# Performance work log

Hardware: AMD Instinct MI355X
Metric: run time of the kernel (lower is better)

Reference implementation:

```python
import jax, jax.numpy as jnp
import numpy as np

EPS = 1e-8


def setup_inputs() -> dict:
    key = jax.random.key(0)
    k1, k2, k3, k4, k5 = jax.random.split(key, 5)
    B, N_LOG, N_PHYS, E = 16, 512, 2048, 2048
    P = jax.random.uniform(k1, (B, N_LOG, N_PHYS), dtype=jnp.float32)
    d_hw = jax.random.randint(k2, (N_PHYS, N_PHYS), 0, 4, dtype=jnp.int32)
    edge_src = jax.random.randint(k3, (B, E), 0, N_LOG, dtype=jnp.int32)
    edge_dst = jax.random.randint(k4, (B, E), 0, N_LOG, dtype=jnp.int32)
    edge_w = jax.random.uniform(k5, (B, E), dtype=jnp.float32)
    return {"P": P, "d_hw": d_hw, "edge_src": edge_src,
            "edge_dst": edge_dst, "edge_w": edge_w}


def reference(P, d_hw, edge_src, edge_dst, edge_w):
    # A_hw[p,q] = 1 where hardware distance == 1 (adjacent qubits)
    A_hw = (d_hw == 1).astype(P.dtype)                      # [Q, Q]
    B = P.shape[0]
    # Dense contraction once per batch: PA[b,i,q] = sum_p P[b,i,p] A[p,q]
    PA = jnp.einsum('bip,pq->biq', P, A_hw)                 # [B, N, Q]
    b_idx = jnp.arange(B)[:, None]                          # [B, 1]
    gi = PA[b_idx, edge_src]                                # [B, E, Q]
    gj = P[b_idx, edge_dst]                                 # [B, E, Q]
    adj_score = jnp.einsum('beq,beq->be', gi, gj)           # [B, E]
    sample_adj = jnp.sum(edge_w * adj_score, axis=-1)       # [B]
    sample_weight = jnp.maximum(jnp.sum(edge_w, axis=-1), EPS)
    # every sample has edges -> valid_samples = B
    loss = -jnp.mean(sample_adj / sample_weight)
    return loss
```

## Files before the change

### kernel.cpp

```cpp
#include <hip/hip_runtime.h>
#include <hip/hip_bf16.h>

#define BATCH 16
#define NLOG 512
#define Q 2048
#define NEDGE 2048
#define M_TOT (BATCH * NLOG)
#define KB 2048

typedef float f32x4 __attribute__((ext_vector_type(4)));
typedef int i32x4 __attribute__((ext_vector_type(4)));
typedef int i32x8 __attribute__((ext_vector_type(8)));

__device__ __forceinline__ unsigned char to_e4m3(float f) {
    int pk = __builtin_amdgcn_cvt_pk_fp8_f32(f, f, 0, false);
    return (unsigned char)(pk & 0xff);
}

__global__ __launch_bounds__(256) void prep(const float* __restrict__ P,
                                            unsigned char* __restrict__ P8,
                                            const int* __restrict__ d_hw,
                                            unsigned char* __restrict__ A8t,
                                            unsigned* __restrict__ counter) {
    int bid = blockIdx.x;
    if (bid == 0 && threadIdx.x == 0) *counter = 0u;
    if (bid < 8192) {
        int i = (bid * 256 + threadIdx.x) * 8;
        float4 v0 = *(const float4*)(P + i);
        float4 v1 = *(const float4*)(P + i + 4);
        int lo = 0, hi = 0;
        lo = __builtin_amdgcn_cvt_pk_fp8_f32(v0.x, v0.y, lo, false);
        lo = __builtin_amdgcn_cvt_pk_fp8_f32(v0.z, v0.w, lo, true);
        hi = __builtin_amdgcn_cvt_pk_fp8_f32(v1.x, v1.y, hi, false);
        hi = __builtin_amdgcn_cvt_pk_fp8_f32(v1.z, v1.w, hi, true);
        int2 st; st.x = lo; st.y = hi;
        *(int2*)(P8 + i) = st;
    } else {
        bid -= 8192;
        __shared__ unsigned char tile[32][33];
        int q0 = (bid & 63) * 32;
        int p0 = (bid >> 6) * 32;
        int tx = threadIdx.x & 31;
        int ty = threadIdx.x >> 5;
        for (int s = 0; s < 32; s += 8) {
            int p = p0 + ty + s;
            int v = d_hw[(size_t)p * Q + q0 + tx];
            tile[ty + s][tx] = (v == 1) ? 0x38 : 0x00;
        }
        __syncthreads();
        for (int s = 0; s < 32; s += 8) {
            A8t[(size_t)(q0 + ty + s) * Q + p0 + tx] = tile[tx][ty + s];
        }
    }
}

__global__ __launch_bounds__(256, 2) void gemm_bt8(const unsigned char* __restrict__ A,
                                                   const unsigned char* __restrict__ Bt,
                                                   unsigned char* __restrict__ PA8) {
    __shared__ unsigned char As[32768];
    __shared__ unsigned char Bs[16384];

    const int t = threadIdx.x;
    const int w = t >> 6;
    const int wr = w >> 1, wc = w & 1;
    const int l = t & 63;
    const int quad = l >> 4;
    const int lane16 = l & 15;

    const int m0 = blockIdx.x * 256;
    const int n0 = blockIdx.y * 128;

    const int s_row = t >> 3;
    const int s_off = (((t & 7) ^ (s_row & 7)) << 4);

    const int r7 = lane16 & 7;
    const int c0 = ((2 * quad) ^ r7) << 4;
    const int c1 = ((2 * quad + 1) ^ r7) << 4;

    f32x4 acc[8][4] = {};

    for (int k0 = 0; k0 < KB; k0 += 128) {
        #pragma unroll
        for (int c = 0; c < 8; c++) {
            const unsigned char* g = A + (size_t)(m0 + c * 32 + s_row) * KB + k0 + s_off;
            __builtin_amdgcn_global_load_lds(
                (const __attribute__((address_space(1))) void*)g,
                (__attribute__((address_space(3))) void*)(As + c * 4096 + w * 1024),
                16, 0, 0);
        }
        #pragma unroll
        for (int c = 0; c < 4; c++) {
            const unsigned char* g = Bt + (size_t)(n0 + c * 32 + s_row) * KB + k0 + s_off;
            __builtin_amdgcn_global_load_lds(
                (const __attribute__((address_space(1))) void*)g,
                (__attribute__((address_space(3))) void*)(Bs + c * 4096 + w * 1024),
                16, 0, 0);
        }
        __syncthreads();

        i32x8 bfr[4];
        #pragma unroll
        for (int j = 0; j < 4; j++) {
            int base = (wc * 64 + j * 16 + lane16) << 7;
            i32x4 lo = *(const i32x4*)(Bs + base + c0);
            i32x4 hi = *(const i32x4*)(Bs + base + c1);
            bfr[j] = __builtin_shufflevector(lo, hi, 0, 1, 2, 3, 4, 5, 6, 7);
        }
        #pragma unroll
        for (int i = 0; i < 8; i++) {
            int base = (wr * 128 + i * 16 + lane16) << 7;
            i32x4 lo = *(const i32x4*)(As + base + c0);
            i32x4 hi = *(const i32x4*)(As + base + c1);
            i32x8 af = __builtin_shufflevector(lo, hi, 0, 1, 2, 3, 4, 5, 6, 7);
            #pragma unroll
            for (int j = 0; j < 4; j++)
                acc[i][j] = __builtin_amdgcn_mfma_scale_f32_16x16x128_f8f6f4(
                    af, bfr[j], acc[i][j], 0, 0,
                    0, 127,
                    0, 127);
        }
        __syncthreads();
    }

    #pragma unroll
    for (int i = 0; i < 8; i++) {
        #pragma unroll
        for (int j = 0; j < 4; j++) {
            #pragma unroll
            for (int r = 0; r < 4; r++) {
                int row = m0 + wr * 128 + i * 16 + quad * 4 + r;
                int col = n0 + wc * 64 + j * 16 + lane16;
                PA8[(size_t)row * Q + col] = to_e4m3(acc[i][j][r] * (1.0f / 256.0f));
            }
        }
    }
}

__global__ __launch_bounds__(256, 2) void gemm_s8(const unsigned char* __restrict__ PA8,
                                                  const unsigned char* __restrict__ P8,
                                                  __hip_bfloat16* __restrict__ S) {
    __shared__ unsigned char As[8192];
    __shared__ unsigned char Bs[16384];

    const int t = threadIdx.x;
    const int w = t >> 6;
    const int wr = w >> 1, wc = w & 1;
    const int l = t & 63;
    const int quad = l >> 4;
    const int lane16 = l & 15;

    const int b = blockIdx.z;
    const int m0 = blockIdx.x * 64;
    const int n0 = blockIdx.y * 128;
    const unsigned char* A  = PA8 + (size_t)b * NLOG * Q;
    const unsigned char* Bt = P8  + (size_t)b * NLOG * Q;
    __hip_bfloat16* C = S + (size_t)b * NLOG * NLOG;

    const int s_row = t >> 3;
    const int s_off = (((t & 7) ^ (s_row & 7)) << 4);
    const int r7 = lane16 & 7;
    const int c0 = ((2 * quad) ^ r7) << 4;
    const int c1 = ((2 * quad + 1) ^ r7) << 4;

    f32x4 acc[2][4] = {};

    for (int k0 = 0; k0 < KB; k0 += 128) {
        #pragma unroll
        for (int c = 0; c < 2; c++) {
            const unsigned char* g = A + (size_t)(m0 + c * 32 + s_row) * KB + k0 + s_off;
            __builtin_amdgcn_global_load_lds(
                (const __attribute__((address_space(1))) void*)g,
                (__attribute__((address_space(3))) void*)(As + c * 4096 + w * 1024),
                16, 0, 0);
        }
        #pragma unroll
        for (int c = 0; c < 4; c++) {
            const unsigned char* g = Bt + (size_t)(n0 + c * 32 + s_row) * KB + k0 + s_off;
            __builtin_amdgcn_global_load_lds(
                (const __attribute__((address_space(1))) void*)g,
                (__attribute__((address_space(3))) void*)(Bs + c * 4096 + w * 1024),
                16, 0, 0);
        }
        __syncthreads();

        i32x8 bfr[4];
        #pragma unroll
        for (int j = 0; j < 4; j++) {
            int base = (wc * 64 + j * 16 + lane16) << 7;
            i32x4 lo = *(const i32x4*)(Bs + base + c0);
            i32x4 hi = *(const i32x4*)(Bs + base + c1);
            bfr[j] = __builtin_shufflevector(lo, hi, 0, 1, 2, 3, 4, 5, 6, 7);
        }
        #pragma unroll
        for (int i = 0; i < 2; i++) {
            int base = (wr * 32 + i * 16 + lane16) << 7;
            i32x4 lo = *(const i32x4*)(As + base + c0);
            i32x4 hi = *(const i32x4*)(As + base + c1);
            i32x8 af = __builtin_shufflevector(lo, hi, 0, 1, 2, 3, 4, 5, 6, 7);
            #pragma unroll
            for (int j = 0; j < 4; j++)
                acc[i][j] = __builtin_amdgcn_mfma_scale_f32_16x16x128_f8f6f4(
                    af, bfr[j], acc[i][j], 0, 0, 0, 127, 0, 127);
        }
        __syncthreads();
    }

    #pragma unroll
    for (int i = 0; i < 2; i++) {
        #pragma unroll
        for (int j = 0; j < 4; j++) {
            #pragma unroll
            for (int r = 0; r < 4; r++) {
                int row = m0 + wr * 32 + i * 16 + quad * 4 + r;
                int col = n0 + wc * 64 + j * 16 + lane16;
                C[(size_t)row * NLOG + col] = __float2bfloat16(acc[i][j][r]);
            }
        }
    }
}

__global__ __launch_bounds__(256) void edge_final(const __hip_bfloat16* __restrict__ S,
                                                  const int* __restrict__ esrc,
                                                  const int* __restrict__ edst,
                                                  const float* __restrict__ ew,
                                                  float* __restrict__ adj,
                                                  float* __restrict__ wsum,
                                                  unsigned* __restrict__ counter,
                                                  float* __restrict__ out) {
    const int b = blockIdx.x;
    const int t = threadIdx.x;
    const unsigned short* Sb = (const unsigned short*)S + (size_t)b * NLOG * NLOG;
    float a = 0.f, ws = 0.f;
    #pragma unroll
    for (int k = 0; k < NEDGE / 256; k++) {
        int e = b * NEDGE + k * 256 + t;
        int src = esrc[e];
        int dst = edst[e];
        float wg = ew[e];
        float s = __uint_as_float((unsigned)Sb[src * NLOG + dst] << 16) * 256.0f;
        a += wg * s;
        ws += wg;
    }
    #pragma unroll
    for (int off = 32; off > 0; off >>= 1) {
        a += __shfl_xor(a, off);
        ws += __shfl_xor(ws, off);
    }
    __shared__ float ra[4], rw[4];
    if ((t & 63) == 0) { ra[t >> 6] = a; rw[t >> 6] = ws; }
    __syncthreads();

    __shared__ unsigned done;
    if (t == 0) {
        atomicExch(&adj[b],  ra[0] + ra[1] + ra[2] + ra[3]);
        atomicExch(&wsum[b], rw[0] + rw[1] + rw[2] + rw[3]);
        __threadfence();
        done = atomicAdd(counter, 1u);
    }
    __syncthreads();
    if (done == BATCH - 1 && t == 0) {
        __threadfence();
        float s = 0.f;
        #pragma unroll
        for (int bb = 0; bb < BATCH; bb++) {
            float av = atomicAdd(&adj[bb], 0.0f);
            float wv = atomicAdd(&wsum[bb], 0.0f);
            s += av / fmaxf(wv, 1e-8f);
        }
        out[0] = -s / (float)BATCH;
    }
}

extern "C" void kernel_launch(void* const* d_in, const int* in_sizes, int n_in,
                              void* d_out, int out_size, void* d_ws, size_t ws_size,
                              hipStream_t stream) {
    const float* P    = (const float*)d_in[0];
    const int* d_hw   = (const int*)d_in[1];
    const int* esrc   = (const int*)d_in[2];
    const int* edst   = (const int*)d_in[3];
    const float* ew   = (const float*)d_in[4];
    float* out        = (float*)d_out;

    char* ws = (char*)d_ws;
    unsigned char* P8  = (unsigned char*)ws;
    unsigned char* A8t = (unsigned char*)(ws + 16777216);
    unsigned char* PA8 = (unsigned char*)(ws + 20971520);
    __hip_bfloat16* S  = (__hip_bfloat16*)(ws + 37748736);
    float* adj         = (float*)(ws + 46137344);
    float* wsum        = (float*)(ws + 46137344 + 64);
    unsigned* counter  = (unsigned*)(ws + 46137344 + 128);

    prep<<<8192 + 4096, 256, 0, stream>>>(P, P8, d_hw, A8t, counter);
    gemm_bt8<<<dim3(M_TOT / 256, Q / 128), 256, 0, stream>>>(P8, A8t, PA8);
    gemm_s8<<<dim3(NLOG / 64, NLOG / 128, BATCH), 256, 0, stream>>>(PA8, P8, S);
    edge_final<<<BATCH, 256, 0, stream>>>(S, esrc, edst, ew, adj, wsum, counter, out);
}
```

Before: 183.1 us.

## Replace dense per-batch S GEMM with direct per-edge gathered dot products

Drops the full 512x512 per-batch S = PA·Pᵀ GEMM and the S buffer. Each edge now gathers its PA row and P row and computes their dot product on the fp8 MFMA, keeping only the diagonal of each 16x16 output tile. Blocks accumulate into adj/wsum with atomicAdd, and the last of 512 blocks computes the final loss. This removes the N²·Q GEMM work in exchange for about 2x redundant row gathers per edge and diagonal-only MFMA use.

```diff
diff --git a/kernel.cpp b/kernel.cpp
--- a/kernel.cpp
+++ b/kernel.cpp
@@ -21,9 +21,14 @@
                                             unsigned char* __restrict__ P8,
                                             const int* __restrict__ d_hw,
                                             unsigned char* __restrict__ A8t,
+                                            float* __restrict__ adj,
+                                            float* __restrict__ wsum,
                                             unsigned* __restrict__ counter) {
     int bid = blockIdx.x;
-    if (bid == 0 && threadIdx.x == 0) *counter = 0u;
+    if (bid == 0) {
+        if (threadIdx.x == 0) *counter = 0u;
+        if (threadIdx.x < BATCH) { adj[threadIdx.x] = 0.f; wsum[threadIdx.x] = 0.f; }
+    }
     if (bid < 8192) {
         int i = (bid * 256 + threadIdx.x) * 8;
         float4 v0 = *(const float4*)(P + i);
@@ -136,129 +141,77 @@
     }
 }
 
-__global__ __launch_bounds__(256, 2) void gemm_s8(const unsigned char* __restrict__ PA8,
-                                                  const unsigned char* __restrict__ P8,
-                                                  __hip_bfloat16* __restrict__ S) {
-    __shared__ unsigned char As[8192];
-    __shared__ unsigned char Bs[16384];
-
+__global__ __launch_bounds__(256, 2) void edge_dot(const unsigned char* __restrict__ PA8,
+                                                   const unsigned char* __restrict__ P8,
+                                                   const int* __restrict__ esrc,
+                                                   const int* __restrict__ edst,
+                                                   const float* __restrict__ ew,
+                                                   float* __restrict__ adj,
+                                                   float* __restrict__ wsum,
+                                                   unsigned* __restrict__ counter,
+                                                   float* __restrict__ out) {
+    const int lid = blockIdx.x;
+    const int b   = (lid & 7) | ((lid >> 8) << 3);
+    const int bx  = (lid >> 3) & 31;
     const int t = threadIdx.x;
     const int w = t >> 6;
-    const int wr = w >> 1, wc = w & 1;
-    const int l = t & 63;
-    const int quad = l >> 4;
-    const int lane16 = l & 15;
-
-    const int b = blockIdx.z;
-    const int m0 = blockIdx.x * 64;
-    const int n0 = blockIdx.y * 128;
-    const unsigned char* A  = PA8 + (size_t)b * NLOG * Q;
-    const unsigned char* Bt = P8  + (size_t)b * NLOG * Q;
-    __hip_bfloat16* C = S + (size_t)b * NLOG * NLOG;
-
-    const int s_row = t >> 3;
-    const int s_off = (((t & 7) ^ (s_row & 7)) << 4);
-    const int r7 = lane16 & 7;
-    const int c0 = ((2 * quad) ^ r7) << 4;
-    const int c1 = ((2 * quad + 1) ^ r7) << 4;
-
-    f32x4 acc[2][4] = {};
-
-    for (int k0 = 0; k0 < KB; k0 += 128) {
-        #pragma unroll
-        for (int c = 0; c < 2; c++) {
-            const unsigned char* g = A + (size_t)(m0 + c * 32 + s_row) * KB + k0 + s_off;
-            __builtin_amdgcn_global_load_lds(
-                (const __attribute__((address_space(1))) void*)g,
-                (__attribute__((address_space(3))) void*)(As + c * 4096 + w * 1024),
-                16, 0, 0);
-        }
-        #pragma unroll
-        for (int c = 0; c < 4; c++) {
-            const unsigned char* g = Bt + (size_t)(n0 + c * 32 + s_row) * KB + k0 + s_off;
-            __builtin_amdgcn_global_load_lds(
-                (const __attribute__((address_space(1))) void*)g,
-                (__attribute__((address_space(3))) void*)(Bs + c * 4096 + w * 1024),
-                16, 0, 0);
-        }
-        __syncthreads();
-
-        i32x8 bfr[4];
-        #pragma unroll
-        for (int j = 0; j < 4; j++) {
-            int base = (wc * 64 + j * 16 + lane16) << 7;
-            i32x4 lo = *(const i32x4*)(Bs + base + c0);
-            i32x4 hi = *(const i32x4*)(Bs + base + c1);
-            bfr[j] = __builtin_shufflevector(lo, hi, 0, 1, 2, 3, 4, 5, 6, 7);
-        }
-        #pragma unroll
-        for (int i = 0; i < 2; i++) {
-            int base = (wr * 32 + i * 16 + lane16) << 7;
-            i32x4 lo = *(const i32x4*)(As + base + c0);
-            i32x4 hi = *(const i32x4*)(As + base + c1);
-            i32x8 af = __builtin_shufflevector(lo, hi, 0, 1, 2, 3, 4, 5, 6, 7);
-            #pragma unroll
-            for (int j = 0; j < 4; j++)
-                acc[i][j] = __builtin_amdgcn_mfma_scale_f32_16x16x128_f8f6f4(
-                    af, bfr[j], acc[i][j], 0, 0, 0, 127, 0, 127);
-        }
-        __syncthreads();
-    }
-
-    #pragma unroll
-    for (int i = 0; i < 2; i++) {
-        #pragma unroll
-        for (int j = 0; j < 4; j++) {
-            #pragma unroll
-            for (int r = 0; r < 4; r++) {
-                int row = m0 + wr * 32 + i * 16 + quad * 4 + r;
-                int col = n0 + wc * 64 + j * 16 + lane16;
-                C[(size_t)row * NLOG + col] = __float2bfloat16(acc[i][j][r]);
-            }
-        }
-    }
-}
-
-__global__ __launch_bounds__(256) void edge_final(const __hip_bfloat16* __restrict__ S,
-                                                  const int* __restrict__ esrc,
-                                                  const int* __restrict__ edst,
-                                                  const float* __restrict__ ew,
-                                                  float* __restrict__ adj,
-                                                  float* __restrict__ wsum,
-                                                  unsigned* __restrict__ counter,
-                                                  float* __restrict__ out) {
-    const int b = blockIdx.x;
-    const int t = threadIdx.x;
-    const unsigned short* Sb = (const unsigned short*)S + (size_t)b * NLOG * NLOG;
-    float a = 0.f, ws = 0.f;
-    #pragma unroll
-    for (int k = 0; k < NEDGE / 256; k++) {
-        int e = b * NEDGE + k * 256 + t;
-        int src = esrc[e];
-        int dst = edst[e];
-        float wg = ew[e];
-        float s = __uint_as_float((unsigned)Sb[src * NLOG + dst] << 16) * 256.0f;
-        a += wg * s;
-        ws += wg;
-    }
+    const int lane = t & 63;
+    const int lane16 = lane & 15;
+    const int quad = lane >> 4;
+
+    const int eg = b * NEDGE + bx * 64 + w * 16 + lane16;
+    const int src = esrc[eg];
+    const int dst = edst[eg];
+    const float we = ew[eg];
+
+    const unsigned char* ap = PA8 + (size_t)(b * NLOG + src) * Q + quad * 32;
+    const unsigned char* bp = P8  + (size_t)(b * NLOG + dst) * Q + quad * 32;
+
+    f32x4 acc0 = {}, acc1 = {};
+    #pragma unroll 2
+    for (int k0 = 0; k0 < KB; k0 += 256) {
+        i32x4 a0l = *(const i32x4*)(ap + k0);
+        i32x4 a0h = *(const i32x4*)(ap + k0 + 16);
+        i32x4 b0l = *(const i32x4*)(bp + k0);
+        i32x4 b0h = *(const i32x4*)(bp + k0 + 16);
+        i32x4 a1l = *(const i32x4*)(ap + k0 + 128);
+        i32x4 a1h = *(const i32x4*)(ap + k0 + 144);
+        i32x4 b1l = *(const i32x4*)(bp + k0 + 128);
+        i32x4 b1h = *(const i32x4*)(bp + k0 + 144);
+        acc0 = __builtin_amdgcn_mfma_scale_f32_16x16x128_f8f6f4(
+            __builtin_shufflevector(a0l, a0h, 0, 1, 2, 3, 4, 5, 6, 7),
+            __builtin_shufflevector(b0l, b0h, 0, 1, 2, 3, 4, 5, 6, 7),
+            acc0, 0, 0, 0, 127, 0, 127);
+        acc1 = __builtin_amdgcn_mfma_scale_f32_16x16x128_f8f6f4(
+            __builtin_shufflevector(a1l, a1h, 0, 1, 2, 3, 4, 5, 6, 7),
+            __builtin_shufflevector(b1l, b1h, 0, 1, 2, 3, 4, 5, 6, 7),
+            acc1, 0, 0, 0, 127, 0, 127);
+    }
+    f32x4 accs = acc0 + acc1;
+
+    const int r = lane16 & 3;
+    float d = (r == 0) ? accs[0] : (r == 1) ? accs[1] : (r == 2) ? accs[2] : accs[3];
+    float contrib = ((lane16 >> 2) == quad) ? we * d * 256.0f : 0.0f;
+    float wpart = (quad == 0) ? we : 0.0f;
     #pragma unroll
     for (int off = 32; off > 0; off >>= 1) {
-        a += __shfl_xor(a, off);
-        ws += __shfl_xor(ws, off);
-    }
+        contrib += __shfl_xor(contrib, off);
+        wpart   += __shfl_xor(wpart, off);
+    }
+
     __shared__ float ra[4], rw[4];
-    if ((t & 63) == 0) { ra[t >> 6] = a; rw[t >> 6] = ws; }
+    if (lane == 0) { ra[w] = contrib; rw[w] = wpart; }
     __syncthreads();
 
     __shared__ unsigned done;
     if (t == 0) {
-        atomicExch(&adj[b],  ra[0] + ra[1] + ra[2] + ra[3]);
-        atomicExch(&wsum[b], rw[0] + rw[1] + rw[2] + rw[3]);
+        atomicAdd(&adj[b],  ra[0] + ra[1] + ra[2] + ra[3]);
+        atomicAdd(&wsum[b], rw[0] + rw[1] + rw[2] + rw[3]);
         __threadfence();
         done = atomicAdd(counter, 1u);
     }
     __syncthreads();
-    if (done == BATCH - 1 && t == 0) {
+    if (t == 0 && done == 512 - 1) {
         __threadfence();
         float s = 0.f;
         #pragma unroll
@@ -285,13 +238,11 @@
     unsigned char* P8  = (unsigned char*)ws;
     unsigned char* A8t = (unsigned char*)(ws + 16777216);
     unsigned char* PA8 = (unsigned char*)(ws + 20971520);
-    __hip_bfloat16* S  = (__hip_bfloat16*)(ws + 37748736);
-    float* adj         = (float*)(ws + 46137344);
-    float* wsum        = (float*)(ws + 46137344 + 64);
-    unsigned* counter  = (unsigned*)(ws + 46137344 + 128);
-
-    prep<<<8192 + 4096, 256, 0, stream>>>(P, P8, d_hw, A8t, counter);
+    float* adj         = (float*)(ws + 37748736);
+    float* wsum        = (float*)(ws + 37748736 + 64);
+    unsigned* counter  = (unsigned*)(ws + 37748736 + 128);
+
+    prep<<<8192 + 4096, 256, 0, stream>>>(P, P8, d_hw, A8t, adj, wsum, counter);
     gemm_bt8<<<dim3(M_TOT / 256, Q / 128), 256, 0, stream>>>(P8, A8t, PA8);
-    gemm_s8<<<dim3(NLOG / 64, NLOG / 128, BATCH), 256, 0, stream>>>(PA8, P8, S);
-    edge_final<<<BATCH, 256, 0, stream>>>(S, esrc, edst, ew, adj, wsum, counter, out);
-}
+    edge_dot<<<512, 256, 0, stream>>>(PA8, P8, esrc, edst, ew, adj, wsum, counter, out);
+}
```

New measurement: 179.8 us. Within noise of the previous version (-1.8%).
